# Kernel tuning notes

Hardware: AMD Instinct MI355X
Metric: run time of the kernel (lower is better)

## Reference

```python
import jax, jax.numpy as jnp
import numpy as np

CRIT = 15          # critical_dimension
GAMMA = 0.2        # gamma_param
DELTA = 0.03       # delta_param
THETA_NC = 1e-35   # theta_noncomm
MAXD = 100         # max_dimension


def _build_theta(dim):
    i = jnp.arange(dim)
    # theta[i,j] = theta_nc * (-1)^(i+j) for j>i, antisymmetric, zero diag
    sign = jnp.where(((i[:, None] + i[None, :]) % 2) == 0, 1.0, -1.0)
    antisym = jnp.sign(i[None, :] - i[:, None]).astype(jnp.float32)
    return (THETA_NC * sign * antisym).astype(jnp.float32)


def setup_inputs() -> dict:
    key = jax.random.key(0)
    k1, k2 = jax.random.split(key)
    B, IN = 4096, 100
    x = jax.random.uniform(k1, (B, IN), dtype=jnp.float32)
    W = jax.random.normal(k2, (MAXD, MAXD), dtype=jnp.float32)
    theta = _build_theta(MAXD)
    return {"x": x, "inner_coefficients": W, "theta_matrix": theta, "dimension": 100}


def _forward(x, W, theta, dimension):
    B, IN = x.shape
    D = int(dimension)
    P = min(IN, D)

    # ---- inner functions phi_{q,p}(x_p), vectorized over (q, p) ----
    q = jnp.arange(D, dtype=jnp.float32)
    k = q + 1.0
    # superconvergence factor S_q (only used for q >= CRIT; where() guards q<CRIT)
    S = 1.0 + GAMMA * jnp.log(q / CRIT) * (1.0 - jnp.exp(-DELTA * (q - CRIT)))
    coeff = jnp.where(q < CRIT, 1.0 / k, 1.0 / (k * S))          # [D]
    exp_term = jnp.exp(-DELTA * k * k)                            # [D]
    sin_term = jnp.sin(jnp.pi * k[None, :, None] * x[:, None, :P])  # [B,D,P]
    inner_p = (coeff * exp_term)[None, :, None] * sin_term * W[:D, :P][None]
    inner = jnp.pad(inner_p, ((0, 0), (0, 0), (0, IN - P)))      # [B,D,IN], zero pad like torch

    # ---- outer functions: Chebyshev recurrence on mean(tanh(sum_p inner)) ----
    x_norm = jnp.tanh(inner.sum(-1))          # [B,D]
    x_mean = jnp.mean(x_norm, axis=-1)        # [B]
    N = 2 * D + 1
    T0 = jnp.ones_like(x_mean)
    T1 = x_mean

    def cheb_step(carry, _):
        tm2, tm1 = carry
        tn = 2.0 * x_mean * tm1 - tm2
        return (tm1, tn), tn

    _, rest = jax.lax.scan(cheb_step, (T0, T1), None, length=N - 2)  # [N-2, B]
    outer = jnp.concatenate([T0[:, None], T1[:, None], rest.T], axis=1)  # [B, 2D+1]

    # ---- noncommutative composition (Moyal-Weyl star product) ----
    inner_mean = inner.mean(-1)                 # [B,D]
    product = outer[:, :D] * inner_mean         # [B,D]
    R = min(D, theta.shape[0], IN)
    th = theta[:R, :R]
    # sum_{mu!=nu} (inner_mu - inner_nu) * theta[mu,nu]  (diag(theta)=0)
    grad_sum = jnp.einsum('bqm,m->bq', inner[:, :, :R], th.sum(1) - th.sum(0))
    # correction = Re(0.5j * grad_sum); grad_sum is real, so the real part is 0
    corr = 0.0 * grad_sum
    return product + corr


def reference(x, inner_coefficients, theta_matrix, dimension):
    return _forward(x, inner_coefficients, theta_matrix, dimension)
```

## Files before the change

### kernel.cpp

```cpp
#include <hip/hip_runtime.h>
#include <math.h>


#define IN_DIM 100
#define MAXD   100
#define NP4    (IN_DIM / 4)
#define WAVES  16
#define BLK    (WAVES * 64)
#define ROWS   WAVES
#define INV2PI 0.15915494309189535f

__device__ __forceinline__ float fast_tanh(float v) {
    float e = __expf(2.0f * v);
    return 1.0f - 2.0f / (e + 1.0f);
}

__global__ __launch_bounds__(BLK) void kat_kernel(
    const float* __restrict__ x, const float* __restrict__ W,
    const int* __restrict__ dimp, float* __restrict__ out, int B)
{
    const int D = *dimp;
    const int P = (IN_DIM < D) ? IN_DIM : D;

    __shared__ float4 cwA[NP4][64];
    __shared__ float4 cwB[NP4][64];

    const int t = threadIdx.x;
    const int row0 = blockIdx.x * ROWS;

    for (int idx = t; idx < NP4 * 128; idx += BLK) {
        int p4 = idx >> 7;
        int q  = idx & 127;
        float4 v = make_float4(0.f, 0.f, 0.f, 0.f);
        if (q < MAXD && q < D) {
            float k = (float)(q + 1);
            float c;
            if (q < 15) {
                c = 1.0f / k;
            } else {
                float qf = (float)q;
                float S = 1.0f + 0.2f * __logf(qf / 15.0f) * (1.0f - __expf(-0.03f * (qf - 15.0f)));
                c = 1.0f / (k * S);
            }
            c *= __expf(-0.03f * k * k);
            float4 wv = ((const float4*)W)[q * (MAXD / 4) + p4];
            int p = 4 * p4;
            v.x = (p     < P) ? c * wv.x : 0.0f;
            v.y = (p + 1 < P) ? c * wv.y : 0.0f;
            v.z = (p + 2 < P) ? c * wv.z : 0.0f;
            v.w = (p + 3 < P) ? c * wv.w : 0.0f;
        }
        if (q < 64) cwA[p4][q]      = v;
        else        cwB[p4][q - 64] = v;
    }
    __syncthreads();

    const int w    = t >> 6;
    const int lane = t & 63;
    const int b    = row0 + w;

    const int bu = __builtin_amdgcn_readfirstlane((b < B) ? b : (B - 1));
    const float4* __restrict__ xb4 = (const float4*)(x + (size_t)bu * IN_DIM);

    const int q0 = lane;
    const int q1 = lane + 64;

    const float f0 = 0.5f * (float)(q0 + 1);
    const float f1 = 0.5f * (float)(q1 + 1);

    float a0 = 0.0f, a1 = 0.0f;
    for (int p4 = 0; p4 < NP4; ++p4) {
        float4 xv = xb4[p4];
        float4 c0 = cwA[p4][lane];
        float4 c1 = cwB[p4][lane];

        a0 = fmaf(__builtin_amdgcn_sinf(f0 * xv.x), c0.x, a0);
        a1 = fmaf(__builtin_amdgcn_sinf(f1 * xv.x), c1.x, a1);
        a0 = fmaf(__builtin_amdgcn_sinf(f0 * xv.y), c0.y, a0);
        a1 = fmaf(__builtin_amdgcn_sinf(f1 * xv.y), c1.y, a1);
        a0 = fmaf(__builtin_amdgcn_sinf(f0 * xv.z), c0.z, a0);
        a1 = fmaf(__builtin_amdgcn_sinf(f1 * xv.z), c1.z, a1);
        a0 = fmaf(__builtin_amdgcn_sinf(f0 * xv.w), c0.w, a0);
        a1 = fmaf(__builtin_amdgcn_sinf(f1 * xv.w), c1.w, a1);
    }

    float s = fast_tanh(a0) + fast_tanh(a1);
    #pragma unroll
    for (int m = 32; m; m >>= 1) s += __shfl_xor(s, m);

    const float thr = acosf(s / (float)D) * INV2PI;
    const float inv = 1.0f / (float)IN_DIM;
    if (b < B) {
        if (q0 < D) out[b * D + q0] = __builtin_amdgcn_cosf((float)q0 * thr) * a0 * inv;
        if (q1 < D) out[b * D + q1] = __builtin_amdgcn_cosf((float)q1 * thr) * a1 * inv;
    }
}

extern "C" void kernel_launch(void* const* d_in, const int* in_sizes, int n_in,
                              void* d_out, int out_size, void* d_ws, size_t ws_size,
                              hipStream_t stream) {
    const float* x    = (const float*)d_in[0];
    const float* W    = (const float*)d_in[1];
    const int*   dimp = (const int*)d_in[3];
    float*       out  = (float*)d_out;

    const int B = in_sizes[0] / IN_DIM;
    const int grid = (B + ROWS - 1) / ROWS;

    hipLaunchKernelGGL(kat_kernel, dim3(grid), dim3(BLK), 0, stream,
                       x, W, dimp, out, B);
}
```

Baseline: 15.02 us.

## Split each row's q range across two waves with shared-memory reduction

Each batch row is now handled by two waves, each covering 64 of the q outputs, where before one wave computed both halves. The block holds 8 rows instead of 16, so the grid doubles. Per-half tanh sums are combined through shared memory after a block-wide barrier. This shortens the per-wave dependent sin/FMA chain and adds parallelism, at the cost of an extra __syncthreads and twice as many per-block coefficient-table setups.

Result: no change. 14.76 us (-1.7%).

```diff
diff --git a/kernel.cpp b/kernel.cpp
--- a/kernel.cpp
+++ b/kernel.cpp
@@ -5,9 +5,8 @@
 #define IN_DIM 100
 #define MAXD   100
 #define NP4    (IN_DIM / 4)
-#define WAVES  16
-#define BLK    (WAVES * 64)
-#define ROWS   WAVES
+#define BLK    1024
+#define ROWSB  8
 #define INV2PI 0.15915494309189535f
 
 __device__ __forceinline__ float fast_tanh(float v) {
@@ -22,11 +21,11 @@
     const int D = *dimp;
     const int P = (IN_DIM < D) ? IN_DIM : D;
 
-    __shared__ float4 cwA[NP4][64];
-    __shared__ float4 cwB[NP4][64];
+    __shared__ float4 cw[NP4][128];
+    __shared__ float  rowsum[ROWSB][2];
 
     const int t = threadIdx.x;
-    const int row0 = blockIdx.x * ROWS;
+    const int row0 = blockIdx.x * ROWSB;
 
     for (int idx = t; idx < NP4 * 128; idx += BLK) {
         int p4 = idx >> 7;
@@ -50,50 +49,44 @@
             v.z = (p + 2 < P) ? c * wv.z : 0.0f;
             v.w = (p + 3 < P) ? c * wv.w : 0.0f;
         }
-        if (q < 64) cwA[p4][q]      = v;
-        else        cwB[p4][q - 64] = v;
+        cw[p4][q] = v;
     }
     __syncthreads();
 
     const int w    = t >> 6;
     const int lane = t & 63;
-    const int b    = row0 + w;
+    const int r    = w & (ROWSB - 1);
+    const int half = w >> 3;
+    const int b    = row0 + r;
 
     const int bu = __builtin_amdgcn_readfirstlane((b < B) ? b : (B - 1));
     const float4* __restrict__ xb4 = (const float4*)(x + (size_t)bu * IN_DIM);
 
-    const int q0 = lane;
-    const int q1 = lane + 64;
+    const int   qi = lane + (half << 6);
+    const float f  = 0.5f * (float)(qi + 1);
 
-    const float f0 = 0.5f * (float)(q0 + 1);
-    const float f1 = 0.5f * (float)(q1 + 1);
-
-    float a0 = 0.0f, a1 = 0.0f;
+    float a = 0.0f;
     for (int p4 = 0; p4 < NP4; ++p4) {
         float4 xv = xb4[p4];
-        float4 c0 = cwA[p4][lane];
-        float4 c1 = cwB[p4][lane];
+        float4 c  = cw[p4][qi];
 
-        a0 = fmaf(__builtin_amdgcn_sinf(f0 * xv.x), c0.x, a0);
-        a1 = fmaf(__builtin_amdgcn_sinf(f1 * xv.x), c1.x, a1);
-        a0 = fmaf(__builtin_amdgcn_sinf(f0 * xv.y), c0.y, a0);
-        a1 = fmaf(__builtin_amdgcn_sinf(f1 * xv.y), c1.y, a1);
-        a0 = fmaf(__builtin_amdgcn_sinf(f0 * xv.z), c0.z, a0);
-        a1 = fmaf(__builtin_amdgcn_sinf(f1 * xv.z), c1.z, a1);
-        a0 = fmaf(__builtin_amdgcn_sinf(f0 * xv.w), c0.w, a0);
-        a1 = fmaf(__builtin_amdgcn_sinf(f1 * xv.w), c1.w, a1);
+        a = fmaf(__builtin_amdgcn_sinf(f * xv.x), c.x, a);
+        a = fmaf(__builtin_amdgcn_sinf(f * xv.y), c.y, a);
+        a = fmaf(__builtin_amdgcn_sinf(f * xv.z), c.z, a);
+        a = fmaf(__builtin_amdgcn_sinf(f * xv.w), c.w, a);
     }
 
-    float s = fast_tanh(a0) + fast_tanh(a1);
+    float s = fast_tanh(a);
     #pragma unroll
     for (int m = 32; m; m >>= 1) s += __shfl_xor(s, m);
+    if (lane == 0) rowsum[r][half] = s;
+    __syncthreads();
 
-    const float thr = acosf(s / (float)D) * INV2PI;
+    const float tot = rowsum[r][0] + rowsum[r][1];
+    const float thr = acosf(tot / (float)D) * INV2PI;
     const float inv = 1.0f / (float)IN_DIM;
-    if (b < B) {
-        if (q0 < D) out[b * D + q0] = __builtin_amdgcn_cosf((float)q0 * thr) * a0 * inv;
-        if (q1 < D) out[b * D + q1] = __builtin_amdgcn_cosf((float)q1 * thr) * a1 * inv;
-    }
+    if (b < B && qi < D)
+        out[b * D + qi] = __builtin_amdgcn_cosf((float)qi * thr) * a * inv;
 }
 
 extern "C" void kernel_launch(void* const* d_in, const int* in_sizes, int n_in,
@@ -105,7 +98,7 @@
     float*       out  = (float*)d_out;
 
     const int B = in_sizes[0] / IN_DIM;
-    const int grid = (B + ROWS - 1) / ROWS;
+    const int grid = (B + ROWSB - 1) / ROWSB;
 
     hipLaunchKernelGGL(kat_kernel, dim3(grid), dim3(BLK), 0, stream,
                        x, W, dimp, out, B);
```
